# Kernel tuning notes

Measured on AMD Instinct MI355X. Metric: run time of the kernel, lower is better.

The kernel has to match this reference:

```python
import jax, jax.numpy as jnp
import numpy as np

N_NODES = 100000


def gcn_conv(x, src, dst, W, b):
    # PyG GCNConv: linear transform first, then symmetric-normalized aggregation.
    h = x @ W  # [N, out]
    ones = jnp.ones(dst.shape[0], dtype=x.dtype)
    deg = jax.ops.segment_sum(ones, dst, num_segments=N_NODES)  # in-degree incl. self-loops
    dinv = jnp.where(deg > 0, jax.lax.rsqrt(deg), 0.0)
    norm = dinv[src] * dinv[dst]  # [E]
    msg = h[src] * norm[:, None]  # gather + scale
    out = jax.ops.segment_sum(msg, dst, num_segments=N_NODES)  # scatter-add
    return out + b


def add_self_loops(edge_index):
    loops = jnp.arange(N_NODES, dtype=edge_index.dtype)
    src = jnp.concatenate([edge_index[0], loops])
    dst = jnp.concatenate([edge_index[1], loops])
    return src, dst


def setup_inputs() -> dict:
    key = jax.random.key(0)
    k1, k2, k3, k4 = jax.random.split(key, 4)
    N, F, H, C, E = N_NODES, 512, 16, 40, 3200000
    x = jax.random.normal(k1, (N, F), dtype=jnp.float32)
    edge_index = jax.random.randint(k2, (2, E), 0, N, dtype=jnp.int64)
    W1 = jax.random.normal(k3, (F, H), dtype=jnp.float32) * (1.0 / np.sqrt(F))
    b1 = jnp.zeros((H,), dtype=jnp.float32)
    W2 = jax.random.normal(k4, (H, C), dtype=jnp.float32) * (1.0 / np.sqrt(H))
    b2 = jnp.zeros((C,), dtype=jnp.float32)
    return {"x": x, "edge_index": edge_index, "W1": W1, "b1": b1, "W2": W2, "b2": b2}


def reference(x, edge_index, W1, b1, W2, b2):
    src, dst = add_self_loops(edge_index)
    h = gcn_conv(x, src, dst, W1, b1)
    h = jax.nn.relu(h)
    logits = gcn_conv(h, src, dst, W2, b2)
    return jax.nn.log_softmax(logits, axis=1), logits
```

## Files before the change

kernel.cpp:

```cpp
#include <hip/hip_runtime.h>
#include <hip/hip_bf16.h>
#include <math.h>

#define N_NODES 100000
#define F_IN 512
#define H_DIM 16
#define C_DIM 40

#define BSHIFT 9
#define BNODES 512
#define NBUCK 196
#define CHUNK 8192
#define SRC_MASK 0x1FFFF


__global__ void __launch_bounds__(256) bhist_kernel(const int* __restrict__ dst,
                                                    int* __restrict__ BC, int E) {
    __shared__ int cnt[NBUCK];
    int start = blockIdx.x * CHUNK;
    int end = start + CHUNK < E ? start + CHUNK : E;
    for (int i = threadIdx.x; i < NBUCK; i += 256) cnt[i] = 0;
    __syncthreads();
    for (int i = start + threadIdx.x; i < end; i += 256)
        atomicAdd(&cnt[dst[i] >> BSHIFT], 1);
    __syncthreads();
    for (int i = threadIdx.x; i < NBUCK; i += 256) {
        int c = cnt[i];
        if (c) atomicAdd(&BC[i], c);
    }
}


__global__ void __launch_bounds__(256) bscan_kernel(const int* __restrict__ BC,
                                                    int* __restrict__ BO,
                                                    int* __restrict__ cursor,
                                                    int* __restrict__ R, int E, int N) {
    __shared__ int buf[2][256];
    int tid = threadIdx.x;
    int v = (tid < NBUCK) ? BC[tid] : 0;
    int cur = 0;
    buf[0][tid] = v;
    __syncthreads();
    for (int off = 1; off < 256; off <<= 1) {
        int t = buf[cur][tid] + ((tid >= off) ? buf[cur][tid - off] : 0);
        cur ^= 1;
        buf[cur][tid] = t;
        __syncthreads();
    }
    int excl = buf[cur][tid] - v;
    if (tid <= NBUCK) {
        BO[tid] = excl;
        if (tid < NBUCK) cursor[tid] = excl;
    }
    if (tid == 0) R[N] = E;
}


__global__ void __launch_bounds__(256) partition_kernel(const int* __restrict__ src,
                                                        const int* __restrict__ dst,
                                                        int* __restrict__ cursor,
                                                        int* __restrict__ packed, int E) {
    __shared__ int cnt[NBUCK];
    __shared__ int base[NBUCK];
    int start = blockIdx.x * CHUNK;
    int end = start + CHUNK < E ? start + CHUNK : E;
    for (int i = threadIdx.x; i < NBUCK; i += 256) cnt[i] = 0;
    __syncthreads();
    for (int i = start + threadIdx.x; i < end; i += 256)
        atomicAdd(&cnt[dst[i] >> BSHIFT], 1);
    __syncthreads();
    for (int i = threadIdx.x; i < NBUCK; i += 256) {
        int c = cnt[i];
        base[i] = c ? atomicAdd(&cursor[i], c) : 0;
        cnt[i] = 0;
    }
    __syncthreads();
    for (int i = start + threadIdx.x; i < end; i += 256) {
        int d = dst[i];
        int b = d >> BSHIFT;
        int p = base[b] + atomicAdd(&cnt[b], 1);
        packed[p] = ((d & (BNODES - 1)) << 17) | src[i];
    }
}


__global__ void __launch_bounds__(512) sort2_kernel(const int* __restrict__ BO,
                                                    const int* __restrict__ packed,
                                                    int* __restrict__ R,
                                                    float* __restrict__ dinv,
                                                    int* __restrict__ eidx, int N) {
    __shared__ int cnt[BNODES];
    __shared__ int buf[2][BNODES];
    int b = blockIdx.x;
    int tid = threadIdx.x;
    int lo = BO[b], hi = BO[b + 1];
    cnt[tid] = 0;
    __syncthreads();
    for (int e = lo + tid; e < hi; e += 512)
        atomicAdd(&cnt[packed[e] >> 17], 1);
    __syncthreads();
    int deg = cnt[tid];
    int cur = 0;
    buf[0][tid] = deg;
    __syncthreads();
    for (int off = 1; off < 512; off <<= 1) {
        int t = buf[cur][tid] + ((tid >= off) ? buf[cur][tid - off] : 0);
        cur ^= 1;
        buf[cur][tid] = t;
        __syncthreads();
    }
    int excl = lo + buf[cur][tid] - deg;
    int n = (b << BSHIFT) + tid;
    if (n < N) {
        R[n] = excl;
        dinv[n] = rsqrtf((float)(deg + 1));
    }
    cnt[tid] = excl;
    __syncthreads();
    for (int e = lo + tid; e < hi; e += 512) {
        int p = packed[e];
        int pos = atomicAdd(&cnt[p >> 17], 1);
        eidx[pos] = p & SRC_MASK;
    }
}


__global__ void __launch_bounds__(256) gemm1_kernel(const float* __restrict__ x,
                                                    const float* __restrict__ W1,
                                                    const float* __restrict__ dinv,
                                                    float* __restrict__ g1, int N) {
    __shared__ float w[F_IN * H_DIM];
    {
        float4* w4s = (float4*)w;
        const float4* W4 = (const float4*)W1;
        for (int i = threadIdx.x; i < F_IN * H_DIM / 4; i += 256) w4s[i] = W4[i];
    }
    __syncthreads();
    int row = blockIdx.x * 256 + threadIdx.x;
    if (row >= N) return;
    const float4* xr = (const float4*)(x + (size_t)row * F_IN);
    float acc[H_DIM];
#pragma unroll
    for (int k = 0; k < H_DIM; k++) acc[k] = 0.0f;
    const float4* w4 = (const float4*)w;
    for (int f4 = 0; f4 < F_IN / 4; ++f4) {
        float4 xv = xr[f4];
        float xs[4] = {xv.x, xv.y, xv.z, xv.w};
#pragma unroll
        for (int q = 0; q < 4; q++) {
            float wq[H_DIM];
#pragma unroll
            for (int p = 0; p < 4; p++) *(float4*)&wq[4 * p] = w4[(f4 * 4 + q) * 4 + p];
            float s = xs[q];
#pragma unroll
            for (int k = 0; k < H_DIM; k++) acc[k] += s * wq[k];
        }
    }
    float di = dinv[row];
    float4* o = (float4*)(g1 + (size_t)row * H_DIM);
#pragma unroll
    for (int p = 0; p < 4; p++)
        o[p] = make_float4(acc[4 * p] * di, acc[4 * p + 1] * di,
                           acc[4 * p + 2] * di, acc[4 * p + 3] * di);
}


__global__ void __launch_bounds__(256) agg1_kernel(const int* __restrict__ R,
                                                   const int* __restrict__ eidx,
                                                   const float* __restrict__ g1,
                                                   const float* __restrict__ dinv,
                                                   const float* __restrict__ b1,
                                                   float* __restrict__ g2, int N) {
    int t = blockIdx.x * 256 + threadIdx.x;
    int n = t >> 4;
    if (n >= N) return;
    int k = t & 15;
    int lo = R[n], hi = R[n + 1];
    float sum = g1[t];
    int e = lo;
    for (; e + 8 <= hi; e += 8) {
        int s[8];
        float v[8];
#pragma unroll
        for (int u = 0; u < 8; u++) s[u] = eidx[e + u];
#pragma unroll
        for (int u = 0; u < 8; u++) v[u] = g1[s[u] * H_DIM + k];
#pragma unroll
        for (int u = 0; u < 8; u++) sum += v[u];
    }
    for (; e < hi; ++e) sum += g1[eidx[e] * H_DIM + k];
    float di = dinv[n];
    g2[t] = di * fmaxf(di * sum + b1[k], 0.0f);
}

__global__ void __launch_bounds__(256) agg2_kernel(const int* __restrict__ R,
                                                   const int* __restrict__ eidx,
                                                   const float* __restrict__ g2,
                                                   float* __restrict__ s2, int N) {
    int t = blockIdx.x * 256 + threadIdx.x;
    int n = t >> 4;
    if (n >= N) return;
    int k = t & 15;
    int lo = R[n], hi = R[n + 1];
    float sum = g2[t];
    int e = lo;
    for (; e + 8 <= hi; e += 8) {
        int s[8];
        float v[8];
#pragma unroll
        for (int u = 0; u < 8; u++) s[u] = eidx[e + u];
#pragma unroll
        for (int u = 0; u < 8; u++) v[u] = g2[s[u] * H_DIM + k];
#pragma unroll
        for (int u = 0; u < 8; u++) sum += v[u];
    }
    for (; e < hi; ++e) sum += g2[eidx[e] * H_DIM + k];
    s2[t] = sum;
}


__global__ void __launch_bounds__(256) final_kernel(const float* __restrict__ s2,
                                                    const float* __restrict__ dinv,
                                                    const float* __restrict__ W2,
                                                    const float* __restrict__ b2,
                                                    float* __restrict__ out, int N) {
    __shared__ float w2s[H_DIM * C_DIM];
    __shared__ float b2s[C_DIM];
    __shared__ float stage[256 * 41];
    for (int i = threadIdx.x; i < H_DIM * C_DIM; i += 256) w2s[i] = W2[i];
    if (threadIdx.x < C_DIM) b2s[threadIdx.x] = b2[threadIdx.x];
    __syncthreads();
    int n = blockIdx.x * 256 + threadIdx.x;
    int cn = n < N ? n : 0;
    float di = dinv[cn];
    float v[H_DIM];
    const float4* sv = (const float4*)(s2 + (size_t)cn * H_DIM);
#pragma unroll
    for (int p = 0; p < 4; p++) {
        float4 t = sv[p];
        v[4 * p] = di * t.x; v[4 * p + 1] = di * t.y;
        v[4 * p + 2] = di * t.z; v[4 * p + 3] = di * t.w;
    }
    float lg[C_DIM];
    float m = -1e30f;
    for (int c = 0; c < C_DIM; c++) {
        float a = b2s[c];
#pragma unroll
        for (int k = 0; k < H_DIM; k++) a += v[k] * w2s[k * C_DIM + c];
        lg[c] = a;
        m = fmaxf(m, a);
    }
    float ssum = 0.0f;
    for (int c = 0; c < C_DIM; c++) ssum += __expf(lg[c] - m);
    float lse = m + __logf(ssum);

    size_t base = (size_t)blockIdx.x * 256 * C_DIM;
    size_t lim = (size_t)N * C_DIM;
    for (int c = 0; c < C_DIM; c++) stage[threadIdx.x * 41 + c] = lg[c] - lse;
    __syncthreads();
    for (int i = threadIdx.x; i < 256 * C_DIM; i += 256) {
        int nn = i / C_DIM, c = i - nn * C_DIM;
        size_t g = base + i;
        if (g < lim) out[g] = stage[nn * 41 + c];
    }
    __syncthreads();
    for (int c = 0; c < C_DIM; c++) stage[threadIdx.x * 41 + c] = lg[c];
    __syncthreads();
    for (int i = threadIdx.x; i < 256 * C_DIM; i += 256) {
        int nn = i / C_DIM, c = i - nn * C_DIM;
        size_t g = base + i;
        if (g < lim) out[lim + g] = stage[nn * 41 + c];
    }
}


extern "C" void kernel_launch(void* const* d_in, const int* in_sizes, int n_in,
                              void* d_out, int out_size, void* d_ws, size_t ws_size,
                              hipStream_t stream) {
    const float* x  = (const float*)d_in[0];
    const int* ei   = (const int*)d_in[1];
    const float* W1 = (const float*)d_in[2];
    const float* b1 = (const float*)d_in[3];
    const float* W2 = (const float*)d_in[4];
    const float* b2 = (const float*)d_in[5];
    float* out = (float*)d_out;

    const int N = N_NODES;
    const int E = in_sizes[1] / 2;
    const int* src = ei;
    const int* dst = ei + E;

    int* R      = (int*)d_ws;
    int* BC     = R + 100016;
    int* BO     = BC + 512;
    int* cursor = BO + 256;
    float* dinv = (float*)(cursor + 256);
    int* eidx   = (int*)(dinv + 100016);
    int* packed = eidx + E;
    float* g1   = (float*)packed;
    float* g2   = g1 + 16 * N;
    float* s2   = g1;

    const int NB = (N + 255) / 256;
    const int NCH = (E + CHUNK - 1) / CHUNK;

    hipMemsetAsync(BC, 0, NBUCK * sizeof(int), stream);
    bhist_kernel<<<NCH, 256, 0, stream>>>(dst, BC, E);
    bscan_kernel<<<1, 256, 0, stream>>>(BC, BO, cursor, R, E, N);
    partition_kernel<<<NCH, 256, 0, stream>>>(src, dst, cursor, packed, E);
    sort2_kernel<<<NBUCK, 512, 0, stream>>>(BO, packed, R, dinv, eidx, N);

    gemm1_kernel<<<NB, 256, 0, stream>>>(x, W1, dinv, g1, N);
    agg1_kernel<<<(N * 16 + 255) / 256, 256, 0, stream>>>(R, eidx, g1, dinv, b1, g2, N);
    agg2_kernel<<<(N * 16 + 255) / 256, 256, 0, stream>>>(R, eidx, g2, s2, N);
    final_kernel<<<NB, 256, 0, stream>>>(s2, dinv, W2, b2, out, N);
}
```

Baseline: 572.2 us.

## Double-buffer x loads in gemm1 and read W1 directly from global

```diff
diff --git a/kernel.cpp b/kernel.cpp
--- a/kernel.cpp
+++ b/kernel.cpp
@@ -125,43 +125,60 @@
 }
 
 
-__global__ void __launch_bounds__(256) gemm1_kernel(const float* __restrict__ x,
-                                                    const float* __restrict__ W1,
-                                                    const float* __restrict__ dinv,
-                                                    float* __restrict__ g1, int N) {
-    __shared__ float w[F_IN * H_DIM];
-    {
-        float4* w4s = (float4*)w;
-        const float4* W4 = (const float4*)W1;
-        for (int i = threadIdx.x; i < F_IN * H_DIM / 4; i += 256) w4s[i] = W4[i];
-    }
-    __syncthreads();
-    int row = blockIdx.x * 256 + threadIdx.x;
-    if (row >= N) return;
-    const float4* xr = (const float4*)(x + (size_t)row * F_IN);
+#define G1_ISSUE(BUF, KC)                                            \
+    {                                                                \
+        _Pragma("unroll")                                            \
+        for (int p = 0; p < 4; ++p) BUF[p] = xr[(KC) * 4 + p];       \
+    }
+
+#define G1_COMPUTE(BUF, KC)                                          \
+    {                                                                \
+        const float4* Wk = (const float4*)(W1 + (KC) * 16 * H_DIM);  \
+        const float* xf = (const float*)BUF;                         \
+        _Pragma("unroll")                                            \
+        for (int j = 0; j < 16; ++j) {                               \
+            float s = xf[j];                                         \
+            _Pragma("unroll")                                        \
+            for (int p = 0; p < 4; ++p) {                            \
+                float4 wv = Wk[j * 4 + p];                           \
+                acc[4 * p + 0] += s * wv.x;                          \
+                acc[4 * p + 1] += s * wv.y;                          \
+                acc[4 * p + 2] += s * wv.z;                          \
+                acc[4 * p + 3] += s * wv.w;                          \
+            }                                                        \
+        }                                                            \
+    }
+
+__global__ void __launch_bounds__(64) gemm1_kernel(const float* __restrict__ x,
+                                                   const float* __restrict__ W1,
+                                                   const float* __restrict__ dinv,
+                                                   float* __restrict__ g1, int N) {
+    int row = blockIdx.x * 64 + threadIdx.x;
+    int cr = row < N ? row : N - 1;
+    const float4* xr = (const float4*)(x + (size_t)cr * F_IN);
+
+    float4 bufA[4], bufB[4];
     float acc[H_DIM];
 #pragma unroll
     for (int k = 0; k < H_DIM; k++) acc[k] = 0.0f;
-    const float4* w4 = (const float4*)w;
-    for (int f4 = 0; f4 < F_IN / 4; ++f4) {
-        float4 xv = xr[f4];
-        float xs[4] = {xv.x, xv.y, xv.z, xv.w};
-#pragma unroll
-        for (int q = 0; q < 4; q++) {
-            float wq[H_DIM];
-#pragma unroll
-            for (int p = 0; p < 4; p++) *(float4*)&wq[4 * p] = w4[(f4 * 4 + q) * 4 + p];
-            float s = xs[q];
-#pragma unroll
-            for (int k = 0; k < H_DIM; k++) acc[k] += s * wq[k];
-        }
-    }
-    float di = dinv[row];
-    float4* o = (float4*)(g1 + (size_t)row * H_DIM);
-#pragma unroll
-    for (int p = 0; p < 4; p++)
-        o[p] = make_float4(acc[4 * p] * di, acc[4 * p + 1] * di,
-                           acc[4 * p + 2] * di, acc[4 * p + 3] * di);
+
+    G1_ISSUE(bufA, 0);
+#pragma unroll
+    for (int kc = 0; kc < F_IN / 16; kc += 2) {
+        G1_ISSUE(bufB, kc + 1);
+        G1_COMPUTE(bufA, kc);
+        if (kc + 2 < F_IN / 16) G1_ISSUE(bufA, kc + 2);
+        G1_COMPUTE(bufB, kc + 1);
+    }
+
+    if (row < N) {
+        float di = dinv[row];
+        float4* o = (float4*)(g1 + (size_t)row * H_DIM);
+#pragma unroll
+        for (int p = 0; p < 4; p++)
+            o[p] = make_float4(acc[4 * p] * di, acc[4 * p + 1] * di,
+                               acc[4 * p + 2] * di, acc[4 * p + 3] * di);
+    }
 }
 
 
@@ -310,7 +327,7 @@
     partition_kernel<<<NCH, 256, 0, stream>>>(src, dst, cursor, packed, E);
     sort2_kernel<<<NBUCK, 512, 0, stream>>>(BO, packed, R, dinv, eidx, N);
 
-    gemm1_kernel<<<NB, 256, 0, stream>>>(x, W1, dinv, g1, N);
+    gemm1_kernel<<<(N + 63) / 64, 64, 0, stream>>>(x, W1, dinv, g1, N);
     agg1_kernel<<<(N * 16 + 255) / 256, 256, 0, stream>>>(R, eidx, g1, dinv, b1, g2, N);
     agg2_kernel<<<(N * 16 + 255) / 256, 256, 0, stream>>>(R, eidx, g2, s2, N);
     final_kernel<<<NB, 256, 0, stream>>>(s2, dinv, W2, b2, out, N);
```

Measured after the change: 534.9 us. 6.5% less time.
